# Optimization experiments

Hardware: AMD Instinct MI355X
Metric: run time of the kernel (lower is better)

Reference implementation:

```python
import jax, jax.numpy as jnp
import numpy as np

N = 50000          # nodes
E = 1600000        # edges (avg degree 32)
H = 64             # hidden dim (module default x=64)
C = 10             # num_classes = max(y)+1
SLOPE = 0.01       # torch leaky_relu default


def _glorot(key, shape):
    lim = jnp.sqrt(6.0 / (shape[0] + shape[1]))
    return jax.random.uniform(key, shape, jnp.float32, -lim, lim)


def setup_inputs() -> dict:
    key = jax.random.key(0)
    ks = jax.random.split(key, 8)
    x = jax.random.normal(ks[0], (N, 1), jnp.float32)
    edge_index = jax.random.randint(ks[1], (2, E), 0, N, dtype=jnp.int64)
    W1 = _glorot(ks[2], (1, 10));  b1 = jnp.zeros((10,), jnp.float32)
    W2 = _glorot(ks[3], (10, H));  b2 = jnp.zeros((H,), jnp.float32)
    W3 = _glorot(ks[4], (H, H));   b3 = jnp.zeros((H,), jnp.float32)
    fcW = _glorot(ks[5], (H * N, C))
    fcb = jnp.zeros((C,), jnp.float32)
    return {"x": x, "edge_index": edge_index, "W1": W1, "b1": b1,
            "W2": W2, "b2": b2, "W3": W3, "b3": b3, "fcW": fcW, "fcb": fcb}


def _gcn_layer(h, W, b, src, dst, norm):
    # GCNConv: out = D^{-1/2} (A + I) D^{-1/2} (h W) + b
    h = h @ W                                   # [N, out]
    msg = h[src] * norm[:, None]                # gather + edge-scale
    agg = jax.ops.segment_sum(msg, dst, num_segments=N)  # scatter-add
    return agg + b


def reference(x, edge_index, W1, b1, W2, b2, W3, b3, fcW, fcb):
    src, dst = edge_index[0], edge_index[1]
    loop = jnp.arange(N, dtype=src.dtype)
    src_all = jnp.concatenate([src, loop])      # add self-loops
    dst_all = jnp.concatenate([dst, loop])
    deg = jax.ops.segment_sum(jnp.ones_like(dst_all, jnp.float32), dst_all,
                              num_segments=N)   # >= 1 due to self-loops
    dinv = jax.lax.rsqrt(deg)
    norm = dinv[src_all] * dinv[dst_all]        # per-edge normalization

    h = jax.nn.leaky_relu(_gcn_layer(x, W1, b1, src_all, dst_all, norm), SLOPE)
    h = jax.nn.leaky_relu(_gcn_layer(h, W2, b2, src_all, dst_all, norm), SLOPE)
    h = jax.nn.leaky_relu(_gcn_layer(h, W3, b3, src_all, dst_all, norm), SLOPE)

    logits = h.reshape(-1) @ fcW + fcb          # [C]
    return jax.nn.softmax(logits, axis=0)
```

## Files before the change

### kernel.cpp

```cpp
#include <hip/hip_runtime.h>
#include <hip/hip_fp16.h>
#include <hip/hip_fp8.h>


constexpr int F1  = 10;
constexpr int F1P = 16;
constexpr int HD  = 64;
constexpr int NC  = 10;
constexpr int LOGIT_BLOCKS = 4096;

constexpr int BSH   = 7;
constexpr int NBC   = 391;
constexpr int BCAPG = 5120;
constexpr int CSTR  = 16;
constexpr int LCAP  = 38;
constexpr int TILE  = 8192;

using f32x4 = __attribute__((ext_vector_type(4))) float;

static __device__ __forceinline__ float lrelu(float v) {
    return v > 0.0f ? v : 0.01f * v;
}

#if defined(__has_builtin)
#if __has_builtin(__builtin_amdgcn_cvt_f32_fp8)
#define FP8_DECODE(w, c) __builtin_amdgcn_cvt_f32_fp8((int)(w), (c))
#endif
#endif
#ifndef FP8_DECODE
static __device__ __forceinline__ float fp8_decode_sw(unsigned w, int c) {
    __hip_fp8_e4m3 t; t.__x = (unsigned char)(w >> (8 * c)); return (float)t;
}
#define FP8_DECODE(w, c) fp8_decode_sw((w), (c))
#endif

static __device__ __forceinline__ unsigned char fp8_encode(float v) {
    __hip_fp8_e4m3 t(v);
    return (unsigned char)t.__x;
}

__global__ void k_bcur(int* __restrict__ bcur, int NB) {
    int b = blockIdx.x * blockDim.x + threadIdx.x;
    if (b < NB) bcur[b * CSTR] = b * BCAPG;
}

__global__ __launch_bounds__(512) void k_bucket(const int* __restrict__ src,
                                                const int* __restrict__ dst,
                                                int* __restrict__ bcur,
                                                unsigned* __restrict__ bpairs, int E) {
    __shared__ unsigned stage[NBC * LCAP];
    __shared__ int lcnt[NBC];
    for (int i = threadIdx.x; i < NBC; i += 512) lcnt[i] = 0;
    __syncthreads();
    int tile0 = blockIdx.x * TILE;
#pragma unroll
    for (int k = 0; k < TILE / 512; ++k) {
        int e = tile0 + k * 512 + threadIdx.x;
        if (e < E) {
            int d = dst[e];
            unsigned pk = (unsigned)src[e] | ((unsigned)(d & 127) << 16);
            int bb = d >> BSH;
            int pos = atomicAdd(&lcnt[bb], 1);
            if (pos < LCAP) stage[bb * LCAP + pos] = pk;
            else {
                int gp = atomicAdd(&bcur[bb * CSTR], 1);
                bpairs[gp] = pk;
            }
        }
    }
    __syncthreads();
    int wid = threadIdx.x >> 6, lane = threadIdx.x & 63;
    for (int bb = wid; bb < NBC; bb += 8) {
        int cntb = min(lcnt[bb], LCAP);
        if (cntb == 0) continue;
        int gp = 0;
        if (lane == 0) gp = atomicAdd(&bcur[bb * CSTR], cntb);
        gp = __shfl(gp, 0, 64);
        for (int i = lane; i < cntb; i += 64) bpairs[gp + i] = stage[bb * LCAP + i];
    }
}

__global__ __launch_bounds__(256) void k_fine(const int* __restrict__ bcur,
                                              const unsigned* __restrict__ bpairs,
                                              const float* __restrict__ x,
                                              unsigned short* __restrict__ csr,
                                              float* __restrict__ dinv,
                                              float* __restrict__ xs,
                                              int* __restrict__ rowbeg,
                                              int* __restrict__ rowend, int N) {
    __shared__ unsigned short lout[BCAPG];
    __shared__ int lcnt[128], lbeg[128];
    int b = blockIdx.x;
    int n0 = b << BSH;
    int nn = min(128, N - n0);
    int base = b * BCAPG;
    int nedges = bcur[b * CSTR] - base;
    for (int i = threadIdx.x; i < nn; i += 256) lcnt[i] = 0;
    __syncthreads();
    for (int i = threadIdx.x; i < nedges; i += 256)
        atomicAdd(&lcnt[(bpairs[base + i] >> 16) & 127], 1);
    __syncthreads();
    if (threadIdx.x == 0) {
        int acc = 0;
        for (int j = 0; j < nn; ++j) { lbeg[j] = acc; acc += lcnt[j]; }
    }
    __syncthreads();
    for (int i = threadIdx.x; i < nn; i += 256) {
        int node = n0 + i;
        float di = rsqrtf(1.0f + (float)lcnt[i]);
        dinv[node]   = di;
        xs[node]     = x[node] * di;
        rowbeg[node] = base + lbeg[i];
        rowend[node] = base + lbeg[i] + lcnt[i];
    }
    __syncthreads();
    for (int i = threadIdx.x; i < nn; i += 256) lcnt[i] = lbeg[i];
    __syncthreads();
    for (int i = threadIdx.x; i < nedges; i += 256) {
        unsigned p = bpairs[base + i];
        int pos = atomicAdd(&lcnt[(p >> 16) & 127], 1);
        lout[pos] = (unsigned short)(p & 0xFFFFu);
    }
    __syncthreads();
    for (int i = threadIdx.x; i < nedges; i += 256) csr[base + i] = lout[i];
}

__global__ void k_l1h1(const int* __restrict__ rowbeg, const int* __restrict__ rowend,
                       const unsigned short* __restrict__ csr,
                       const float* __restrict__ xs, const float* __restrict__ dinv,
                       const float* __restrict__ W1, const float* __restrict__ b1,
                       __half* __restrict__ h1s, int N) {
    int node = (blockIdx.x * blockDim.x + threadIdx.x) >> 6;
    int lane = threadIdx.x & 63;
    if (node >= N) return;
    int lo = rowbeg[node], hi = rowend[node];
    float acc = 0.0f;
    for (int j = lo + lane; j < hi; j += 64) acc += xs[csr[j]];
#pragma unroll
    for (int off = 32; off > 0; off >>= 1) acc += __shfl_xor(acc, off, 64);
    float di = dinv[node];
    float s = di * (acc + xs[node]);
    if (lane < F1P) {
        float h = (lane < F1) ? lrelu(s * W1[lane] + b1[lane]) * di : 0.0f;
        h1s[node * F1P + lane] = __float2half(h);
    }
}

__global__ __launch_bounds__(256, 4) void k_l2h2(const int* __restrict__ rowbeg,
                                                 const int* __restrict__ rowend,
                                                 const unsigned short* __restrict__ csr,
                                                 const __half* __restrict__ h1s,
                                                 const float* __restrict__ dinv,
                                                 const float* __restrict__ W2,
                                                 const float* __restrict__ b2,
                                                 unsigned char* __restrict__ h2s8, int N) {
    __shared__ float awork[4][12];
    int node = (blockIdx.x * blockDim.x + threadIdx.x) >> 6;
    int wid  = threadIdx.x >> 6;
    int lane = threadIdx.x & 63;
    bool valid = node < N;
    float w2r[F1];
#pragma unroll
    for (int k = 0; k < F1; ++k) w2r[k] = W2[k * HD + lane];
    int g = lane >> 3, f2 = lane & 7;
    int lo = 0, deg = 0;
    if (valid) { lo = rowbeg[node]; deg = rowend[node] - lo; }
    int myidx = (lane < deg) ? (int)csr[lo + lane] : 0;
    int nfull = min(deg, 64);
    float a0 = 0.0f, a1 = 0.0f;
#pragma unroll
    for (int j = 0; j < 64; j += 8) {
        if (j >= nfull) break;
        int e = j + g;
        int sn = __shfl(myidx, e, 64);
        if (e < nfull) {
            __half2 hv = *reinterpret_cast<const __half2*>(h1s + sn * F1P + f2 * 2);
            a0 += __low2float(hv);
            a1 += __high2float(hv);
        }
    }
    for (int j = 64; j < deg; j += 8) {
        int e = j + g;
        if (e < deg) {
            int sn = csr[lo + e];
            __half2 hv = *reinterpret_cast<const __half2*>(h1s + sn * F1P + f2 * 2);
            a0 += __low2float(hv);
            a1 += __high2float(hv);
        }
    }
    a0 += __shfl_xor(a0, 8, 64); a0 += __shfl_xor(a0, 16, 64); a0 += __shfl_xor(a0, 32, 64);
    a1 += __shfl_xor(a1, 8, 64); a1 += __shfl_xor(a1, 16, 64); a1 += __shfl_xor(a1, 32, 64);
    if (valid) {
        __half2 hs = *reinterpret_cast<const __half2*>(h1s + node * F1P + f2 * 2);
        a0 += __low2float(hs);
        a1 += __high2float(hs);
    }
    if (g == 0 && f2 < 5)
        *reinterpret_cast<float2*>(&awork[wid][f2 * 2]) = make_float2(a0, a1);
    __syncthreads();
    float4 av0 = *reinterpret_cast<const float4*>(&awork[wid][0]);
    float4 av1 = *reinterpret_cast<const float4*>(&awork[wid][4]);
    float2 av2 = *reinterpret_cast<const float2*>(&awork[wid][8]);
    float S = av0.x * w2r[0] + av0.y * w2r[1] + av0.z * w2r[2] + av0.w * w2r[3]
            + av1.x * w2r[4] + av1.y * w2r[5] + av1.z * w2r[6] + av1.w * w2r[7]
            + av2.x * w2r[8] + av2.y * w2r[9];
    if (valid) {
        float di = dinv[node];
        h2s8[node * HD + lane] = fp8_encode(lrelu(di * S + b2[lane]) * di);
    }
}

__global__ __launch_bounds__(256, 8) void k_l3h3(const int* __restrict__ rowbeg,
                                                 const int* __restrict__ rowend,
                                                 const unsigned short* __restrict__ csr,
                                                 const unsigned char* __restrict__ h2s8,
                                                 const float* __restrict__ dinv,
                                                 const float* __restrict__ W3,
                                                 const float* __restrict__ b3,
                                                 float* __restrict__ h3, int N) {
    __shared__ float awork[4][HD];
    __shared__ float plds[64][20];
    int node = (blockIdx.x * blockDim.x + threadIdx.x) >> 6;
    int wid  = threadIdx.x >> 6;
    int lane = threadIdx.x & 63;
    bool valid = node < N;
    float w3r[16];
#pragma unroll
    for (int j = 0; j < 16; ++j) w3r[j] = W3[(16 * wid + j) * HD + lane];
    int g = lane >> 4, q = lane & 15;
    int lo = 0, deg = 0;
    if (valid) { lo = rowbeg[node]; deg = rowend[node] - lo; }
    int myidx = (lane < deg) ? (int)csr[lo + lane] : 0;
    int nfull = min(deg, 64);
    float a0 = 0.0f, a1 = 0.0f, a2 = 0.0f, a3 = 0.0f;
#pragma unroll
    for (int j = 0; j < 64; j += 4) {
        if (j >= nfull) break;
        int e = j + g;
        int sn = __shfl(myidx, e, 64);
        if (e < nfull) {
            unsigned wv = *reinterpret_cast<const unsigned*>(h2s8 + sn * HD + q * 4);
            a0 += FP8_DECODE(wv, 0);
            a1 += FP8_DECODE(wv, 1);
            a2 += FP8_DECODE(wv, 2);
            a3 += FP8_DECODE(wv, 3);
        }
    }
    for (int j = 64; j < deg; j += 4) {
        int e = j + g;
        if (e < deg) {
            int sn = csr[lo + e];
            unsigned wv = *reinterpret_cast<const unsigned*>(h2s8 + sn * HD + q * 4);
            a0 += FP8_DECODE(wv, 0);
            a1 += FP8_DECODE(wv, 1);
            a2 += FP8_DECODE(wv, 2);
            a3 += FP8_DECODE(wv, 3);
        }
    }
    a0 += __shfl_xor(a0, 16, 64); a0 += __shfl_xor(a0, 32, 64);
    a1 += __shfl_xor(a1, 16, 64); a1 += __shfl_xor(a1, 32, 64);
    a2 += __shfl_xor(a2, 16, 64); a2 += __shfl_xor(a2, 32, 64);
    a3 += __shfl_xor(a3, 16, 64); a3 += __shfl_xor(a3, 32, 64);
    if (valid) {
        unsigned ws = *reinterpret_cast<const unsigned*>(h2s8 + node * HD + q * 4);
        a0 += FP8_DECODE(ws, 0);
        a1 += FP8_DECODE(ws, 1);
        a2 += FP8_DECODE(ws, 2);
        a3 += FP8_DECODE(ws, 3);
    }
    if (g == 0)
        *reinterpret_cast<float4*>(&awork[wid][q * 4]) = make_float4(a0, a1, a2, a3);
    __syncthreads();
#pragma unroll
    for (int n = 0; n < 4; ++n) {
        float p = 0.0f;
#pragma unroll
        for (int jj = 0; jj < 4; ++jj) {
            float4 av = *reinterpret_cast<const float4*>(&awork[n][16 * wid + 4 * jj]);
            p += av.x * w3r[4 * jj]     + av.y * w3r[4 * jj + 1]
               + av.z * w3r[4 * jj + 2] + av.w * w3r[4 * jj + 3];
        }
        plds[lane][n * 4 + wid] = p;
    }
    __syncthreads();
    if (valid) {
        float4 pv = *reinterpret_cast<const float4*>(&plds[lane][wid * 4]);
        float S = (pv.x + pv.y) + (pv.z + pv.w);
        float di = dinv[node];
        h3[node * HD + lane] = lrelu(di * S + b3[lane]);
    }
}

__global__ __launch_bounds__(256) void k_logits_part(const float* __restrict__ h3,
                                                     const f32x4* __restrict__ fw4,
                                                     float* __restrict__ partial,
                                                     int P ) {
    __shared__ f32x4 stage[1280];
    float acc[NC];
#pragma unroll
    for (int c = 0; c < NC; ++c) acc[c] = 0.0f;
    for (int pbase = blockIdx.x * 256; pbase < P; pbase += gridDim.x * 256) {
        int nfl = min(256, P - pbase) * 5;
        __syncthreads();
        for (int i = threadIdx.x; i < nfl; i += 256)
            stage[i] = __builtin_nontemporal_load(&fw4[(size_t)pbase * 5 + i]);
        __syncthreads();
        int p = pbase + threadIdx.x;
        if (p < P) {
            const f32x4* w = &stage[threadIdx.x * 5];
            f32x4 w0 = w[0], w1 = w[1], w2 = w[2], w3 = w[3], w4 = w[4];
            float2 hv = *reinterpret_cast<const float2*>(h3 + 2 * (size_t)p);
            acc[0] += hv.x * w0.x; acc[1] += hv.x * w0.y; acc[2] += hv.x * w0.z; acc[3] += hv.x * w0.w;
            acc[4] += hv.x * w1.x; acc[5] += hv.x * w1.y; acc[6] += hv.x * w1.z; acc[7] += hv.x * w1.w;
            acc[8] += hv.x * w2.x; acc[9] += hv.x * w2.y; acc[0] += hv.y * w2.z; acc[1] += hv.y * w2.w;
            acc[2] += hv.y * w3.x; acc[3] += hv.y * w3.y; acc[4] += hv.y * w3.z; acc[5] += hv.y * w3.w;
            acc[6] += hv.y * w4.x; acc[7] += hv.y * w4.y; acc[8] += hv.y * w4.z; acc[9] += hv.y * w4.w;
        }
    }
#pragma unroll
    for (int c = 0; c < NC; ++c) {
        float v = acc[c];
#pragma unroll
        for (int off = 32; off > 0; off >>= 1) v += __shfl_down(v, off, 64);
        acc[c] = v;
    }
    __shared__ float ls[4][NC];
    int wid = threadIdx.x >> 6, lane = threadIdx.x & 63;
    if (lane == 0) {
#pragma unroll
        for (int c = 0; c < NC; ++c) ls[wid][c] = acc[c];
    }
    __syncthreads();
    if (threadIdx.x < NC) {
        float ssum = ls[0][threadIdx.x] + ls[1][threadIdx.x]
                   + ls[2][threadIdx.x] + ls[3][threadIdx.x];
        partial[blockIdx.x * NC + threadIdx.x] = ssum;
    }
}

__global__ __launch_bounds__(1024) void k_final(const float* __restrict__ partial, int nblk,
                                                const float* __restrict__ fcb,
                                                float* __restrict__ out) {
    __shared__ float ls[NC];
    if (threadIdx.x < NC) ls[threadIdx.x] = 0.0f;
    __syncthreads();
    const int NCHUNK = 1024 / NC;
    int c = threadIdx.x % NC;
    int chunk = threadIdx.x / NC;
    float ssum = 0.0f;
    if (chunk < NCHUNK)
        for (int i = chunk; i < nblk; i += NCHUNK) ssum += partial[i * NC + c];
    if (chunk < NCHUNK) atomicAdd(&ls[c], ssum);
    __syncthreads();
    if (threadIdx.x == 0) {
        float l[NC], m = -1e30f;
        for (int k = 0; k < NC; ++k) { l[k] = ls[k] + fcb[k]; m = fmaxf(m, l[k]); }
        float sum = 0.0f;
        for (int k = 0; k < NC; ++k) { l[k] = expf(l[k] - m); sum += l[k]; }
        float inv = 1.0f / sum;
        for (int k = 0; k < NC; ++k) out[k] = l[k] * inv;
    }
}

extern "C" void kernel_launch(void* const* d_in, const int* in_sizes, int n_in,
                              void* d_out, int out_size, void* d_ws, size_t ws_size,
                              hipStream_t stream) {
    const float* x   = (const float*)d_in[0];
    const int*   ei  = (const int*)d_in[1];
    const float* W1  = (const float*)d_in[2];
    const float* b1  = (const float*)d_in[3];
    const float* W2  = (const float*)d_in[4];
    const float* b2  = (const float*)d_in[5];
    const float* W3  = (const float*)d_in[6];
    const float* b3  = (const float*)d_in[7];
    const float* fcW = (const float*)d_in[8];
    const float* fcb = (const float*)d_in[9];
    float* out = (float*)d_out;

    const int N = in_sizes[0];
    const int E = in_sizes[1] / 2;
    const int* src = ei;
    const int* dst = ei + E;
    const int NB = (N + 127) >> BSH;

    char* w = (char*)d_ws;
    auto take = [&](size_t elems) { void* p = w; w += elems * 4; return p; };
    float* dinv    = (float*)take(N);
    int*   rowbeg  = (int*)  take(N);
    int*   rowend  = (int*)  take(N);
    int*   bcur    = (int*)  take((size_t)NB * CSTR);
    unsigned short* csr = (unsigned short*)take((size_t)NB * BCAPG / 2);
    float* xs      = (float*)take(N);
    __half* h1s    = (__half*)take((size_t)N * F1P / 2);
    unsigned char* h2s8 = (unsigned char*)take((size_t)N * HD / 4);
    float* h3      = (float*)take((size_t)N * HD);
    float* partial = xs;
    unsigned* bpairs = (unsigned*)h3;

    const int B = 256;
    auto cdiv = [](long long a, long long b) { return (int)((a + b - 1) / b); };

    k_bcur  <<<cdiv(NB, B), B, 0, stream>>>(bcur, NB);
    k_bucket<<<cdiv(E, TILE), 512, 0, stream>>>(src, dst, bcur, bpairs, E);
    k_fine  <<<NB, 256, 0, stream>>>(bcur, bpairs, x, csr, dinv, xs, rowbeg, rowend, N);

    k_l1h1<<<cdiv((long long)N * 64, B), B, 0, stream>>>(rowbeg, rowend, csr, xs, dinv, W1, b1, h1s, N);
    k_l2h2<<<cdiv((long long)N * 64, B), B, 0, stream>>>(rowbeg, rowend, csr, h1s, dinv, W2, b2, h2s8, N);
    k_l3h3<<<cdiv((long long)N * 64, B), B, 0, stream>>>(rowbeg, rowend, csr, h2s8, dinv, W3, b3, h3, N);

    const int P = (N * HD) / 2;
    k_logits_part<<<LOGIT_BLOCKS, B, 0, stream>>>(h3, (const f32x4*)fcW, partial, P);
    k_final<<<1, 1024, 0, stream>>>(partial, LOGIT_BLOCKS, fcb, out);
}
```

Before: 171.2 us.

## Fuse final softmax into logits kernel, halve layer-1 wavefront width, raise occupancy hint

The final reduction and softmax now run inside the logits kernel: the last block to finish, detected with an atomic counter that k_bcur resets, sums the partials and writes the output. This removes one kernel launch. Layer 1 now gives each node 32 lanes instead of 64, so twice as many nodes fit per wave for the short degree-32 rows. The k_l2h2 launch-bounds occupancy hint rises from 4 to 8, which may force register spilling.

```diff
diff --git a/kernel.cpp b/kernel.cpp
--- a/kernel.cpp
+++ b/kernel.cpp
@@ -39,9 +39,10 @@
     return (unsigned char)t.__x;
 }
 
-__global__ void k_bcur(int* __restrict__ bcur, int NB) {
+__global__ void k_bcur(int* __restrict__ bcur, int* __restrict__ ctr, int NB) {
     int b = blockIdx.x * blockDim.x + threadIdx.x;
     if (b < NB) bcur[b * CSTR] = b * BCAPG;
+    if (b == 0) ctr[0] = 0;
 }
 
 __global__ __launch_bounds__(512) void k_bucket(const int* __restrict__ src,
@@ -125,28 +126,34 @@
     for (int i = threadIdx.x; i < nedges; i += 256) csr[base + i] = lout[i];
 }
 
-__global__ void k_l1h1(const int* __restrict__ rowbeg, const int* __restrict__ rowend,
-                       const unsigned short* __restrict__ csr,
-                       const float* __restrict__ xs, const float* __restrict__ dinv,
-                       const float* __restrict__ W1, const float* __restrict__ b1,
-                       __half* __restrict__ h1s, int N) {
-    int node = (blockIdx.x * blockDim.x + threadIdx.x) >> 6;
-    int lane = threadIdx.x & 63;
-    if (node >= N) return;
-    int lo = rowbeg[node], hi = rowend[node];
+__global__ __launch_bounds__(256) void k_l1h1(const int* __restrict__ rowbeg,
+                                              const int* __restrict__ rowend,
+                                              const unsigned short* __restrict__ csr,
+                                              const float* __restrict__ xs,
+                                              const float* __restrict__ dinv,
+                                              const float* __restrict__ W1,
+                                              const float* __restrict__ b1,
+                                              __half* __restrict__ h1s, int N) {
+    int nid = (blockIdx.x * blockDim.x + threadIdx.x) >> 5;
+    int l32 = threadIdx.x & 31;
+    if (nid >= N) return;
+    int lo = rowbeg[nid], hi = rowend[nid];
     float acc = 0.0f;
-    for (int j = lo + lane; j < hi; j += 64) acc += xs[csr[j]];
-#pragma unroll
-    for (int off = 32; off > 0; off >>= 1) acc += __shfl_xor(acc, off, 64);
-    float di = dinv[node];
-    float s = di * (acc + xs[node]);
-    if (lane < F1P) {
-        float h = (lane < F1) ? lrelu(s * W1[lane] + b1[lane]) * di : 0.0f;
-        h1s[node * F1P + lane] = __float2half(h);
-    }
-}
-
-__global__ __launch_bounds__(256, 4) void k_l2h2(const int* __restrict__ rowbeg,
+    for (int j = lo + l32; j < hi; j += 32) acc += xs[csr[j]];
+    acc += __shfl_xor(acc, 1, 64);
+    acc += __shfl_xor(acc, 2, 64);
+    acc += __shfl_xor(acc, 4, 64);
+    acc += __shfl_xor(acc, 8, 64);
+    acc += __shfl_xor(acc, 16, 64);
+    float di = dinv[nid];
+    float s = di * (acc + xs[nid]);
+    if (l32 < F1P) {
+        float h = (l32 < F1) ? lrelu(s * W1[l32] + b1[l32]) * di : 0.0f;
+        h1s[nid * F1P + l32] = __float2half(h);
+    }
+}
+
+__global__ __launch_bounds__(256, 8) void k_l2h2(const int* __restrict__ rowbeg,
                                                  const int* __restrict__ rowend,
                                                  const unsigned short* __restrict__ csr,
                                                  const __half* __restrict__ h1s,
@@ -294,7 +301,10 @@
 __global__ __launch_bounds__(256) void k_logits_part(const float* __restrict__ h3,
                                                      const f32x4* __restrict__ fw4,
                                                      float* __restrict__ partial,
-                                                     int P ) {
+                                                     int P ,
+                                                     const float* __restrict__ fcb,
+                                                     float* __restrict__ out,
+                                                     int* __restrict__ ctr) {
     __shared__ f32x4 stage[1280];
     float acc[NC];
 #pragma unroll
@@ -336,25 +346,27 @@
                    + ls[2][threadIdx.x] + ls[3][threadIdx.x];
         partial[blockIdx.x * NC + threadIdx.x] = ssum;
     }
-}
-
-__global__ __launch_bounds__(1024) void k_final(const float* __restrict__ partial, int nblk,
-                                                const float* __restrict__ fcb,
-                                                float* __restrict__ out) {
-    __shared__ float ls[NC];
-    if (threadIdx.x < NC) ls[threadIdx.x] = 0.0f;
-    __syncthreads();
-    const int NCHUNK = 1024 / NC;
+    __threadfence();
+    __shared__ int amLast;
+    if (threadIdx.x == 0)
+        amLast = (atomicAdd(ctr, 1) == (int)gridDim.x - 1);
+    __syncthreads();
+    if (!amLast) return;
+    __threadfence();
+    __shared__ float cls[NC];
+    if (threadIdx.x < NC) cls[threadIdx.x] = 0.0f;
+    __syncthreads();
+    const int NCHUNK = 256 / NC;
     int c = threadIdx.x % NC;
     int chunk = threadIdx.x / NC;
-    float ssum = 0.0f;
+    float ssum2 = 0.0f;
     if (chunk < NCHUNK)
-        for (int i = chunk; i < nblk; i += NCHUNK) ssum += partial[i * NC + c];
-    if (chunk < NCHUNK) atomicAdd(&ls[c], ssum);
+        for (int i = chunk; i < (int)gridDim.x; i += NCHUNK) ssum2 += partial[i * NC + c];
+    if (chunk < NCHUNK) atomicAdd(&cls[c], ssum2);
     __syncthreads();
     if (threadIdx.x == 0) {
         float l[NC], m = -1e30f;
-        for (int k = 0; k < NC; ++k) { l[k] = ls[k] + fcb[k]; m = fmaxf(m, l[k]); }
+        for (int k = 0; k < NC; ++k) { l[k] = cls[k] + fcb[k]; m = fmaxf(m, l[k]); }
         float sum = 0.0f;
         for (int k = 0; k < NC; ++k) { l[k] = expf(l[k] - m); sum += l[k]; }
         float inv = 1.0f / sum;
@@ -389,6 +401,7 @@
     int*   rowbeg  = (int*)  take(N);
     int*   rowend  = (int*)  take(N);
     int*   bcur    = (int*)  take((size_t)NB * CSTR);
+    int*   ctr     = (int*)  take(16);
     unsigned short* csr = (unsigned short*)take((size_t)NB * BCAPG / 2);
     float* xs      = (float*)take(N);
     __half* h1s    = (__half*)take((size_t)N * F1P / 2);
@@ -400,15 +413,14 @@
     const int B = 256;
     auto cdiv = [](long long a, long long b) { return (int)((a + b - 1) / b); };
 
-    k_bcur  <<<cdiv(NB, B), B, 0, stream>>>(bcur, NB);
+    k_bcur  <<<cdiv(NB, B), B, 0, stream>>>(bcur, ctr, NB);
     k_bucket<<<cdiv(E, TILE), 512, 0, stream>>>(src, dst, bcur, bpairs, E);
     k_fine  <<<NB, 256, 0, stream>>>(bcur, bpairs, x, csr, dinv, xs, rowbeg, rowend, N);
 
-    k_l1h1<<<cdiv((long long)N * 64, B), B, 0, stream>>>(rowbeg, rowend, csr, xs, dinv, W1, b1, h1s, N);
+    k_l1h1<<<cdiv((long long)N * 32, B), B, 0, stream>>>(rowbeg, rowend, csr, xs, dinv, W1, b1, h1s, N);
     k_l2h2<<<cdiv((long long)N * 64, B), B, 0, stream>>>(rowbeg, rowend, csr, h1s, dinv, W2, b2, h2s8, N);
     k_l3h3<<<cdiv((long long)N * 64, B), B, 0, stream>>>(rowbeg, rowend, csr, h2s8, dinv, W3, b3, h3, N);
 
     const int P = (N * HD) / 2;
-    k_logits_part<<<LOGIT_BLOCKS, B, 0, stream>>>(h3, (const f32x4*)fcW, partial, P);
-    k_final<<<1, 1024, 0, stream>>>(partial, LOGIT_BLOCKS, fcb, out);
-}
+    k_logits_part<<<LOGIT_BLOCKS, B, 0, stream>>>(h3, (const f32x4*)fcW, partial, P, fcb, out, ctr);
+}
```

Measured after the change: 488.7 us. +185.4%, slower.
